# Performance work log

Hardware: AMD Instinct MI355X
Metric: run time of the kernel (lower is better)

Reference implementation:

```python
import jax, jax.numpy as jnp
import numpy as np

B, C_IN, H, W = 16, 16, 256, 256  # B must equal out_channels for the module's broadcast
C_OUT = 16


def setup_inputs() -> dict:
    key = jax.random.key(0)
    k1, k2, k3, k4 = jax.random.split(key, 4)
    return {
        "x_real": jax.random.normal(k1, (B, C_IN, H, W), dtype=jnp.float32),
        "x_imag": jax.random.normal(k2, (B, C_IN, H, W), dtype=jnp.float32),
        "w_real": jax.random.normal(k3, (C_OUT, C_IN, H, W), dtype=jnp.float32),
        "w_imag": jax.random.normal(k4, (C_OUT, C_IN, H, W), dtype=jnp.float32),
    }


def reference(x_real, x_imag, w_real, w_imag):
    # HolographicConv: ifft2(fft2(x) * W).real with complex x and W.
    x = jax.lax.complex(x_real, x_imag)            # (B, C_in, H, W) complex64
    w = jax.lax.complex(w_real, w_imag)            # (C_out, C_in, H, W) complex64
    x_freq = jnp.fft.fft2(x, axes=(-2, -1))
    conv_freq = x_freq * w                          # broadcast: B == C_out, k == H == W
    out = jnp.fft.ifft2(conv_freq, axes=(-2, -1))
    return out.real.astype(jnp.float32)
```

## Files before the change

### kernel.cpp

```cpp
#include <hip/hip_runtime.h>


#define PI_F 3.14159265358979323846f

__device__ __forceinline__ float2 cmul2(float2 a, float2 b){
  return make_float2(a.x*b.x - a.y*b.y, a.x*b.y + a.y*b.x);
}
__device__ __forceinline__ float4 f4add(float4 a, float4 b){
  return make_float4(a.x+b.x, a.y+b.y, a.z+b.z, a.w+b.w);
}
__device__ __forceinline__ float4 f4sub(float4 a, float4 b){
  return make_float4(a.x-b.x, a.y-b.y, a.z-b.z, a.w-b.w);
}
__device__ __forceinline__ float4 mulI (float4 t){ return make_float4(-t.y, t.x, -t.w, t.z); }
__device__ __forceinline__ float4 mulmI(float4 t){ return make_float4( t.y,-t.x,  t.w,-t.z); }
__device__ __forceinline__ float4 cmul_pw(float4 a, float2 w){
  return make_float4(a.x*w.x - a.y*w.y, a.x*w.y + a.y*w.x,
                     a.z*w.x - a.w*w.y, a.z*w.y + a.w*w.x);
}
__device__ __forceinline__ float4 cmul_p4(float4 a, float4 w){
  return make_float4(a.x*w.x - a.y*w.y, a.x*w.y + a.y*w.x,
                     a.z*w.z - a.w*w.w, a.z*w.w + a.w*w.z);
}

__device__ __forceinline__ int SW(int e){ return e ^ (e >> 4); }

template<int DIR>
__device__ __forceinline__ void bfly4p(float4 v[4], float2 w1, float2 w2, float2 w3)
{
  float4 apc = f4add(v[0], v[2]), amc = f4sub(v[0], v[2]);
  float4 bpd = f4add(v[1], v[3]), bmd = f4sub(v[1], v[3]);
  float4 jb  = (DIR > 0) ? mulI(bmd) : mulmI(bmd);
  v[0] = f4add(apc, bpd);
  v[1] = cmul_pw(f4sub(amc, jb), w1);
  v[2] = cmul_pw(f4sub(apc, bpd), w2);
  v[3] = cmul_pw(f4add(amc, jb), w3);
}

template<int DIR>
__device__ __forceinline__ void fft256_p(float4 v[4], float4* scr,
                                         const float2 (&tws)[3][3], int lane)
{
  #pragma unroll
  for (int st = 0; st < 3; ++st) {
    const int s  = 1 << (2*st);
    const int ps = lane & ~(s-1);
    const int q  = lane &  (s-1);
    float2 w1 = tws[st][0], w2 = tws[st][1], w3 = tws[st][2];
    if (DIR < 0) { w1.y = -w1.y; w2.y = -w2.y; w3.y = -w3.y; }
    bfly4p<DIR>(v, w1, w2, w3);
    const int dbase = q + 4*ps;
    __builtin_amdgcn_wave_barrier();
    scr[SW(dbase + 0*s)] = v[0];
    scr[SW(dbase + 1*s)] = v[1];
    scr[SW(dbase + 2*s)] = v[2];
    scr[SW(dbase + 3*s)] = v[3];
    __builtin_amdgcn_wave_barrier();
    v[0] = scr[SW(lane +   0)];
    v[1] = scr[SW(lane +  64)];
    v[2] = scr[SW(lane + 128)];
    v[3] = scr[SW(lane + 192)];
    __builtin_amdgcn_wave_barrier();
  }
  bfly4p<DIR>(v, make_float2(1.f,0.f), make_float2(1.f,0.f), make_float2(1.f,0.f));
}

__device__ __forceinline__ void make_tws(float2 (&tws)[3][3], int lane)
{
  #pragma unroll
  for (int st = 0; st < 3; ++st) {
    const int s  = 1 << (2*st);
    const int ps = lane & ~(s-1);
    float sv, cv;
    sincosf(-2.0f * PI_F * (float)ps / 256.0f, &sv, &cv);
    float2 w1 = make_float2(cv, sv);
    float2 w2 = cmul2(w1, w1);
    float2 w3 = cmul2(w1, w2);
    tws[st][0] = w1; tws[st][1] = w2; tws[st][2] = w3;
  }
}

__global__ __launch_bounds__(256, 4) void k_colfft(const float* __restrict__ xr,
                                                   const float* __restrict__ xi,
                                                   float2* __restrict__ wsT)
{
  __shared__ float4 pool[2304];
  const int tid  = threadIdx.x;
  const int imgl = blockIdx.x >> 4;
  const int v0   = (blockIdx.x & 15) * 16;
  const size_t ib = (size_t)imgl * 65536;
  const int q  = tid & 3;
  const int h0 = tid >> 2;
  #pragma unroll
  for (int t = 0; t < 4; ++t) {
    const int u = h0 + 64*t;
    float4 r4 = *(const float4*)(xr + ib + (size_t)u*256 + v0 + 4*q);
    float4 i4 = *(const float4*)(xi + ib + (size_t)u*256 + v0 + 4*q);
    pool[u*9 + 2*q    ] = make_float4(r4.x, i4.x, r4.y, i4.y);
    pool[u*9 + 2*q + 1] = make_float4(r4.z, i4.z, r4.w, i4.w);
  }
  const int wave = tid >> 6, lane = tid & 63;
  float2 tws[3][3];
  make_tws(tws, lane);
  __syncthreads();
  const int cp1 = wave*2, cp2 = wave*2 + 1;
  float4 v1[4], v2[4];
  #pragma unroll
  for (int r = 0; r < 4; ++r) { v1[r] = pool[(lane + 64*r)*9 + cp1];
                                v2[r] = pool[(lane + 64*r)*9 + cp2]; }
  __syncthreads();
  float4* scr = pool + wave*256;
  fft256_p<1>(v1, scr, tws, lane);
  fft256_p<1>(v2, scr, tws, lane);
  {
    float2* oA = wsT + ib + (size_t)(v0 + 2*cp1)*256;
    float2* oB = oA + 256;
    #pragma unroll
    for (int r = 0; r < 4; ++r) {
      const int l = lane + 64*r;
      oA[l] = make_float2(v1[r].x, v1[r].y);
      oB[l] = make_float2(v1[r].z, v1[r].w);
    }
  }
  {
    float2* oA = wsT + ib + (size_t)(v0 + 2*cp2)*256;
    float2* oB = oA + 256;
    #pragma unroll
    for (int r = 0; r < 4; ++r) {
      const int l = lane + 64*r;
      oA[l] = make_float2(v2[r].x, v2[r].y);
      oB[l] = make_float2(v2[r].z, v2[r].w);
    }
  }
}

__global__ __launch_bounds__(256, 4) void k_rowpass(float2* __restrict__ wsT,
                                                    const float* __restrict__ wr,
                                                    const float* __restrict__ wi,
                                                    int img0)
{
  __shared__ float4 pool[2304];
  const int tid  = threadIdx.x;
  const int imgl = blockIdx.x >> 4;
  const int k0   = (blockIdx.x & 15) * 16;
  const size_t ib = (size_t)imgl * 65536;
  const size_t wb = (size_t)(img0 + imgl) * 65536;
  const int c8 = tid & 7;
  const int h0 = tid >> 3;
  #pragma unroll
  for (int t = 0; t < 8; ++t) {
    const int v = h0 + 32*t;
    pool[v*9 + c8] = *(const float4*)(wsT + ib + (size_t)v*256 + k0 + 2*c8);
  }
  const int wave = tid >> 6, lane = tid & 63;
  float2 tws[3][3];
  make_tws(tws, lane);
  __syncthreads();
  const int cp1 = wave*2, cp2 = wave*2 + 1;
  float4 v1[4], v2[4];
  #pragma unroll
  for (int r = 0; r < 4; ++r) { v1[r] = pool[(lane + 64*r)*9 + cp1];
                                v2[r] = pool[(lane + 64*r)*9 + cp2]; }
  __syncthreads();
  float4* scr = pool + wave*256;
  {
    const size_t bA = wb + (size_t)(k0 + 2*cp1)*256, bB = bA + 256;
    float4 wv[4];
    #pragma unroll
    for (int r = 0; r < 4; ++r) {
      const int l = lane + 64*r;
      wv[r] = make_float4(wr[bA + l], wi[bA + l], wr[bB + l], wi[bB + l]);
    }
    fft256_p<1>(v1, scr, tws, lane);
    #pragma unroll
    for (int r = 0; r < 4; ++r) v1[r] = cmul_p4(v1[r], wv[r]);
    fft256_p<-1>(v1, scr, tws, lane);
  }
  {
    const size_t bA = wb + (size_t)(k0 + 2*cp2)*256, bB = bA + 256;
    float4 wv[4];
    #pragma unroll
    for (int r = 0; r < 4; ++r) {
      const int l = lane + 64*r;
      wv[r] = make_float4(wr[bA + l], wi[bA + l], wr[bB + l], wi[bB + l]);
    }
    fft256_p<1>(v2, scr, tws, lane);
    #pragma unroll
    for (int r = 0; r < 4; ++r) v2[r] = cmul_p4(v2[r], wv[r]);
    fft256_p<-1>(v2, scr, tws, lane);
  }
  __syncthreads();
  #pragma unroll
  for (int r = 0; r < 4; ++r) { pool[(lane + 64*r)*9 + cp1] = v1[r];
                                pool[(lane + 64*r)*9 + cp2] = v2[r]; }
  __syncthreads();
  #pragma unroll
  for (int t = 0; t < 8; ++t) {
    const int v = h0 + 32*t;
    *(float4*)(wsT + ib + (size_t)v*256 + k0 + 2*c8) = pool[v*9 + c8];
  }
}

__global__ __launch_bounds__(256, 6) void k_rowifft(const float2* __restrict__ wsT,
                                                    float* __restrict__ out)
{
  __shared__ float4 pool[1152];
  const int tid  = threadIdx.x;
  const int imgl = blockIdx.x >> 4;
  const int v0   = (blockIdx.x & 15) * 16;
  const size_t ib = (size_t)imgl * 65536;
  const int wave = tid >> 6, lane = tid & 63;
  float2 tws[3][3];
  make_tws(tws, lane);
  float4* scr = pool + wave*256;
  float2* ot  = (float2*)pool;
  const float sc = 1.0f / 65536.0f;
  float2 res[2][4];
  #pragma unroll
  for (int p = 0; p < 2; ++p) {
    const int cp = wave*2 + p;
    const float2* pA = wsT + ib + (size_t)(v0 + 2*cp)*256;
    const float2* pB = pA + 256;
    float4 v[4];
    #pragma unroll
    for (int r = 0; r < 4; ++r) {
      const int l = lane + 64*r;
      float2 a = pA[l], b = pB[l];
      v[r] = make_float4(a.x, a.y, b.x, b.y);
    }
    fft256_p<-1>(v, scr, tws, lane);
    #pragma unroll
    for (int r = 0; r < 4; ++r) res[p][r] = make_float2(v[r].x * sc, v[r].z * sc);
  }
  __syncthreads();
  #pragma unroll
  for (int p = 0; p < 2; ++p)
    #pragma unroll
    for (int r = 0; r < 4; ++r)
      ot[(lane + 64*r)*9 + wave*2 + p] = res[p][r];
  __syncthreads();
  const int c4 = tid & 3, h0 = tid >> 2;
  #pragma unroll
  for (int t = 0; t < 4; ++t) {
    const int u = h0 + 64*t;
    float2 a = ot[u*9 + 2*c4], b = ot[u*9 + 2*c4 + 1];
    *(float4*)(out + ib + (size_t)u*256 + v0 + 4*c4) = make_float4(a.x, a.y, b.x, b.y);
  }
}

extern "C" void kernel_launch(void* const* d_in, const int* in_sizes, int n_in,
                              void* d_out, int out_size, void* d_ws, size_t ws_size,
                              hipStream_t stream)
{
  const float* xr = (const float*)d_in[0];
  const float* xi = (const float*)d_in[1];
  const float* wr = (const float*)d_in[2];
  const float* wi = (const float*)d_in[3];
  float* out = (float*)d_out;

  const int IMG = 256;
  const size_t per_img = (size_t)65536 * sizeof(float2);
  int ipc = (int)(ws_size / per_img);
  if (ipc < 1)   ipc = 1;
  if (ipc > IMG) ipc = IMG;
  float2* wsp = (float2*)d_ws;

  for (int img0 = 0; img0 < IMG; img0 += ipc) {
    const int n = (IMG - img0 < ipc) ? (IMG - img0) : ipc;
    k_colfft <<<dim3(n*16), dim3(256), 0, stream>>>(xr + (size_t)img0*65536,
                                                    xi + (size_t)img0*65536, wsp);
    k_rowpass<<<dim3(n*16), dim3(256), 0, stream>>>(wsp, wr, wi, img0);
    k_rowifft<<<dim3(n*16), dim3(256), 0, stream>>>(wsp, out + (size_t)img0*65536);
  }
}
```

Measured before the change: 180.0 us.

## Interleave two FFT columns per wave with separate scratch and XOR-swizzled transpose

Each wave now runs its two 256-point FFTs interleaved in lockstep, each with its own LDS scratch buffer, instead of running them one after another on a shared buffer. This exposes more independent instructions to hide LDS latency. The padded stride-9 transpose layout becomes an XOR-swizzled stride-8 layout, which shrinks LDS. Only the base twiddle is kept in registers, with w2 and w3 recomputed per stage, and the occupancy hints change to 5 blocks, trading extra ALU work and more LDS in the rowifft kernel for lower register pressure and more ILP.

```diff
diff --git a/kernel.cpp b/kernel.cpp
--- a/kernel.cpp
+++ b/kernel.cpp
@@ -24,6 +24,7 @@
 }
 
 __device__ __forceinline__ int SW(int e){ return e ^ (e >> 4); }
+__device__ __forceinline__ int TC(int u, int c){ return u*8 + (c ^ (u & 7)); }
 
 template<int DIR>
 __device__ __forceinline__ void bfly4p(float4 v[4], float2 w1, float2 w2, float2 w3)
@@ -38,34 +39,40 @@
 }
 
 template<int DIR>
-__device__ __forceinline__ void fft256_p(float4 v[4], float4* scr,
-                                         const float2 (&tws)[3][3], int lane)
+__device__ __forceinline__ void fft256_p2(float4 va[4], float4 vb[4],
+                                          float4* sa, float4* sb,
+                                          const float2 (&tw1)[3], int lane)
 {
   #pragma unroll
   for (int st = 0; st < 3; ++st) {
     const int s  = 1 << (2*st);
     const int ps = lane & ~(s-1);
     const int q  = lane &  (s-1);
-    float2 w1 = tws[st][0], w2 = tws[st][1], w3 = tws[st][2];
-    if (DIR < 0) { w1.y = -w1.y; w2.y = -w2.y; w3.y = -w3.y; }
-    bfly4p<DIR>(v, w1, w2, w3);
+    float2 w1 = tw1[st];
+    if (DIR < 0) w1.y = -w1.y;
+    const float2 w2 = cmul2(w1, w1);
+    const float2 w3 = cmul2(w1, w2);
+    bfly4p<DIR>(va, w1, w2, w3);
+    bfly4p<DIR>(vb, w1, w2, w3);
     const int dbase = q + 4*ps;
     __builtin_amdgcn_wave_barrier();
-    scr[SW(dbase + 0*s)] = v[0];
-    scr[SW(dbase + 1*s)] = v[1];
-    scr[SW(dbase + 2*s)] = v[2];
-    scr[SW(dbase + 3*s)] = v[3];
+    sa[SW(dbase + 0*s)] = va[0];  sb[SW(dbase + 0*s)] = vb[0];
+    sa[SW(dbase + 1*s)] = va[1];  sb[SW(dbase + 1*s)] = vb[1];
+    sa[SW(dbase + 2*s)] = va[2];  sb[SW(dbase + 2*s)] = vb[2];
+    sa[SW(dbase + 3*s)] = va[3];  sb[SW(dbase + 3*s)] = vb[3];
     __builtin_amdgcn_wave_barrier();
-    v[0] = scr[SW(lane +   0)];
-    v[1] = scr[SW(lane +  64)];
-    v[2] = scr[SW(lane + 128)];
-    v[3] = scr[SW(lane + 192)];
+    va[0] = sa[SW(lane +   0)];   vb[0] = sb[SW(lane +   0)];
+    va[1] = sa[SW(lane +  64)];   vb[1] = sb[SW(lane +  64)];
+    va[2] = sa[SW(lane + 128)];   vb[2] = sb[SW(lane + 128)];
+    va[3] = sa[SW(lane + 192)];   vb[3] = sb[SW(lane + 192)];
     __builtin_amdgcn_wave_barrier();
   }
-  bfly4p<DIR>(v, make_float2(1.f,0.f), make_float2(1.f,0.f), make_float2(1.f,0.f));
-}
-
-__device__ __forceinline__ void make_tws(float2 (&tws)[3][3], int lane)
+  const float2 one = make_float2(1.f, 0.f);
+  bfly4p<DIR>(va, one, one, one);
+  bfly4p<DIR>(vb, one, one, one);
+}
+
+__device__ __forceinline__ void make_tw1(float2 (&tw1)[3], int lane)
 {
   #pragma unroll
   for (int st = 0; st < 3; ++st) {
@@ -73,18 +80,15 @@
     const int ps = lane & ~(s-1);
     float sv, cv;
     sincosf(-2.0f * PI_F * (float)ps / 256.0f, &sv, &cv);
-    float2 w1 = make_float2(cv, sv);
-    float2 w2 = cmul2(w1, w1);
-    float2 w3 = cmul2(w1, w2);
-    tws[st][0] = w1; tws[st][1] = w2; tws[st][2] = w3;
-  }
-}
-
-__global__ __launch_bounds__(256, 4) void k_colfft(const float* __restrict__ xr,
+    tw1[st] = make_float2(cv, sv);
+  }
+}
+
+__global__ __launch_bounds__(256, 5) void k_colfft(const float* __restrict__ xr,
                                                    const float* __restrict__ xi,
                                                    float2* __restrict__ wsT)
 {
-  __shared__ float4 pool[2304];
+  __shared__ float4 pool[2048];
   const int tid  = threadIdx.x;
   const int imgl = blockIdx.x >> 4;
   const int v0   = (blockIdx.x & 15) * 16;
@@ -96,50 +100,50 @@
     const int u = h0 + 64*t;
     float4 r4 = *(const float4*)(xr + ib + (size_t)u*256 + v0 + 4*q);
     float4 i4 = *(const float4*)(xi + ib + (size_t)u*256 + v0 + 4*q);
-    pool[u*9 + 2*q    ] = make_float4(r4.x, i4.x, r4.y, i4.y);
-    pool[u*9 + 2*q + 1] = make_float4(r4.z, i4.z, r4.w, i4.w);
+    pool[TC(u, 2*q    )] = make_float4(r4.x, i4.x, r4.y, i4.y);
+    pool[TC(u, 2*q + 1)] = make_float4(r4.z, i4.z, r4.w, i4.w);
   }
   const int wave = tid >> 6, lane = tid & 63;
-  float2 tws[3][3];
-  make_tws(tws, lane);
-  __syncthreads();
-  const int cp1 = wave*2, cp2 = wave*2 + 1;
-  float4 v1[4], v2[4];
-  #pragma unroll
-  for (int r = 0; r < 4; ++r) { v1[r] = pool[(lane + 64*r)*9 + cp1];
-                                v2[r] = pool[(lane + 64*r)*9 + cp2]; }
-  __syncthreads();
-  float4* scr = pool + wave*256;
-  fft256_p<1>(v1, scr, tws, lane);
-  fft256_p<1>(v2, scr, tws, lane);
+  float2 tw1[3];
+  make_tw1(tw1, lane);
+  __syncthreads();
+  const int cpa = wave*2, cpb = wave*2 + 1;
+  float4 va[4], vb[4];
+  #pragma unroll
+  for (int r = 0; r < 4; ++r) { va[r] = pool[TC(lane + 64*r, cpa)];
+                                vb[r] = pool[TC(lane + 64*r, cpb)]; }
+  __syncthreads();
+  float4* sa = pool + wave*512;
+  float4* sb = sa + 256;
+  fft256_p2<1>(va, vb, sa, sb, tw1, lane);
   {
-    float2* oA = wsT + ib + (size_t)(v0 + 2*cp1)*256;
+    float2* oA = wsT + ib + (size_t)(v0 + 2*cpa)*256;
     float2* oB = oA + 256;
     #pragma unroll
     for (int r = 0; r < 4; ++r) {
       const int l = lane + 64*r;
-      oA[l] = make_float2(v1[r].x, v1[r].y);
-      oB[l] = make_float2(v1[r].z, v1[r].w);
+      oA[l] = make_float2(va[r].x, va[r].y);
+      oB[l] = make_float2(va[r].z, va[r].w);
     }
   }
   {
-    float2* oA = wsT + ib + (size_t)(v0 + 2*cp2)*256;
+    float2* oA = wsT + ib + (size_t)(v0 + 2*cpb)*256;
     float2* oB = oA + 256;
     #pragma unroll
     for (int r = 0; r < 4; ++r) {
       const int l = lane + 64*r;
-      oA[l] = make_float2(v2[r].x, v2[r].y);
-      oB[l] = make_float2(v2[r].z, v2[r].w);
+      oA[l] = make_float2(vb[r].x, vb[r].y);
+      oB[l] = make_float2(vb[r].z, vb[r].w);
     }
   }
 }
 
-__global__ __launch_bounds__(256, 4) void k_rowpass(float2* __restrict__ wsT,
+__global__ __launch_bounds__(256, 5) void k_rowpass(float2* __restrict__ wsT,
                                                     const float* __restrict__ wr,
                                                     const float* __restrict__ wi,
                                                     int img0)
 {
-  __shared__ float4 pool[2304];
+  __shared__ float4 pool[2048];
   const int tid  = threadIdx.x;
   const int imgl = blockIdx.x >> 4;
   const int k0   = (blockIdx.x & 15) * 16;
@@ -150,100 +154,90 @@
   #pragma unroll
   for (int t = 0; t < 8; ++t) {
     const int v = h0 + 32*t;
-    pool[v*9 + c8] = *(const float4*)(wsT + ib + (size_t)v*256 + k0 + 2*c8);
+    pool[TC(v, c8)] = *(const float4*)(wsT + ib + (size_t)v*256 + k0 + 2*c8);
   }
   const int wave = tid >> 6, lane = tid & 63;
-  float2 tws[3][3];
-  make_tws(tws, lane);
-  __syncthreads();
-  const int cp1 = wave*2, cp2 = wave*2 + 1;
-  float4 v1[4], v2[4];
-  #pragma unroll
-  for (int r = 0; r < 4; ++r) { v1[r] = pool[(lane + 64*r)*9 + cp1];
-                                v2[r] = pool[(lane + 64*r)*9 + cp2]; }
-  __syncthreads();
-  float4* scr = pool + wave*256;
-  {
-    const size_t bA = wb + (size_t)(k0 + 2*cp1)*256, bB = bA + 256;
-    float4 wv[4];
-    #pragma unroll
-    for (int r = 0; r < 4; ++r) {
-      const int l = lane + 64*r;
-      wv[r] = make_float4(wr[bA + l], wi[bA + l], wr[bB + l], wi[bB + l]);
-    }
-    fft256_p<1>(v1, scr, tws, lane);
-    #pragma unroll
-    for (int r = 0; r < 4; ++r) v1[r] = cmul_p4(v1[r], wv[r]);
-    fft256_p<-1>(v1, scr, tws, lane);
-  }
-  {
-    const size_t bA = wb + (size_t)(k0 + 2*cp2)*256, bB = bA + 256;
-    float4 wv[4];
-    #pragma unroll
-    for (int r = 0; r < 4; ++r) {
-      const int l = lane + 64*r;
-      wv[r] = make_float4(wr[bA + l], wi[bA + l], wr[bB + l], wi[bB + l]);
-    }
-    fft256_p<1>(v2, scr, tws, lane);
-    #pragma unroll
-    for (int r = 0; r < 4; ++r) v2[r] = cmul_p4(v2[r], wv[r]);
-    fft256_p<-1>(v2, scr, tws, lane);
-  }
-  __syncthreads();
-  #pragma unroll
-  for (int r = 0; r < 4; ++r) { pool[(lane + 64*r)*9 + cp1] = v1[r];
-                                pool[(lane + 64*r)*9 + cp2] = v2[r]; }
+  float2 tw1[3];
+  make_tw1(tw1, lane);
+  __syncthreads();
+  const int cpa = wave*2, cpb = wave*2 + 1;
+  float4 va[4], vb[4];
+  #pragma unroll
+  for (int r = 0; r < 4; ++r) { va[r] = pool[TC(lane + 64*r, cpa)];
+                                vb[r] = pool[TC(lane + 64*r, cpb)]; }
+  __syncthreads();
+  const size_t ba = wb + (size_t)(k0 + 2*cpa)*256;
+  const size_t bb = wb + (size_t)(k0 + 2*cpb)*256;
+  float4 wva[4], wvb[4];
+  #pragma unroll
+  for (int r = 0; r < 4; ++r) {
+    const int l = lane + 64*r;
+    wva[r] = make_float4(wr[ba + l], wi[ba + l], wr[ba + 256 + l], wi[ba + 256 + l]);
+    wvb[r] = make_float4(wr[bb + l], wi[bb + l], wr[bb + 256 + l], wi[bb + 256 + l]);
+  }
+  float4* sa = pool + wave*512;
+  float4* sb = sa + 256;
+  fft256_p2<1>(va, vb, sa, sb, tw1, lane);
+  #pragma unroll
+  for (int r = 0; r < 4; ++r) { va[r] = cmul_p4(va[r], wva[r]);
+                                vb[r] = cmul_p4(vb[r], wvb[r]); }
+  fft256_p2<-1>(va, vb, sa, sb, tw1, lane);
+  __syncthreads();
+  #pragma unroll
+  for (int r = 0; r < 4; ++r) { pool[TC(lane + 64*r, cpa)] = va[r];
+                                pool[TC(lane + 64*r, cpb)] = vb[r]; }
   __syncthreads();
   #pragma unroll
   for (int t = 0; t < 8; ++t) {
     const int v = h0 + 32*t;
-    *(float4*)(wsT + ib + (size_t)v*256 + k0 + 2*c8) = pool[v*9 + c8];
-  }
-}
-
-__global__ __launch_bounds__(256, 6) void k_rowifft(const float2* __restrict__ wsT,
+    *(float4*)(wsT + ib + (size_t)v*256 + k0 + 2*c8) = pool[TC(v, c8)];
+  }
+}
+
+__global__ __launch_bounds__(256, 5) void k_rowifft(const float2* __restrict__ wsT,
                                                     float* __restrict__ out)
 {
-  __shared__ float4 pool[1152];
+  __shared__ float4 pool[2048];
   const int tid  = threadIdx.x;
   const int imgl = blockIdx.x >> 4;
   const int v0   = (blockIdx.x & 15) * 16;
   const size_t ib = (size_t)imgl * 65536;
   const int wave = tid >> 6, lane = tid & 63;
-  float2 tws[3][3];
-  make_tws(tws, lane);
-  float4* scr = pool + wave*256;
-  float2* ot  = (float2*)pool;
-  const float sc = 1.0f / 65536.0f;
-  float2 res[2][4];
-  #pragma unroll
-  for (int p = 0; p < 2; ++p) {
-    const int cp = wave*2 + p;
-    const float2* pA = wsT + ib + (size_t)(v0 + 2*cp)*256;
+  float2 tw1[3];
+  make_tw1(tw1, lane);
+  const int cpa = wave*2, cpb = wave*2 + 1;
+  float4 va[4], vb[4];
+  {
+    const float2* pA = wsT + ib + (size_t)(v0 + 2*cpa)*256;
     const float2* pB = pA + 256;
-    float4 v[4];
+    const float2* pC = wsT + ib + (size_t)(v0 + 2*cpb)*256;
+    const float2* pD = pC + 256;
     #pragma unroll
     for (int r = 0; r < 4; ++r) {
       const int l = lane + 64*r;
-      float2 a = pA[l], b = pB[l];
-      v[r] = make_float4(a.x, a.y, b.x, b.y);
+      float2 a = pA[l], b = pB[l], c = pC[l], d = pD[l];
+      va[r] = make_float4(a.x, a.y, b.x, b.y);
+      vb[r] = make_float4(c.x, c.y, d.x, d.y);
     }
-    fft256_p<-1>(v, scr, tws, lane);
-    #pragma unroll
-    for (int r = 0; r < 4; ++r) res[p][r] = make_float2(v[r].x * sc, v[r].z * sc);
-  }
-  __syncthreads();
-  #pragma unroll
-  for (int p = 0; p < 2; ++p)
-    #pragma unroll
-    for (int r = 0; r < 4; ++r)
-      ot[(lane + 64*r)*9 + wave*2 + p] = res[p][r];
+  }
+  float4* sa = pool + wave*512;
+  float4* sb = sa + 256;
+  fft256_p2<-1>(va, vb, sa, sb, tw1, lane);
+  __syncthreads();
+  float2* ot = (float2*)pool;
+  const float sc = 1.0f / 65536.0f;
+  #pragma unroll
+  for (int r = 0; r < 4; ++r) {
+    const int u = lane + 64*r;
+    ot[TC(u, cpa)] = make_float2(va[r].x * sc, va[r].z * sc);
+    ot[TC(u, cpb)] = make_float2(vb[r].x * sc, vb[r].z * sc);
+  }
   __syncthreads();
   const int c4 = tid & 3, h0 = tid >> 2;
   #pragma unroll
   for (int t = 0; t < 4; ++t) {
     const int u = h0 + 64*t;
-    float2 a = ot[u*9 + 2*c4], b = ot[u*9 + 2*c4 + 1];
+    float2 a = ot[TC(u, 2*c4)], b = ot[TC(u, 2*c4 + 1)];
     *(float4*)(out + ib + (size_t)u*256 + v0 + 4*c4) = make_float4(a.x, a.y, b.x, b.y);
   }
 }
```

After: 310.1 us. 1.72x slower.
